# Kernel tuning notes

Hardware: AMD Instinct MI355X
Metric: run time of the kernel (lower is better)

The kernel has to match this reference:

```python
import jax, jax.numpy as jnp
import numpy as np
from jax import lax

B, C, H, W = 2, 64, 64, 64


def _conv1x1(x, w, b):
    # w: [Cout, Cin], x: [B, Cin, H, W]
    return jnp.einsum('oi,bihw->bohw', w, x) + b[None, :, None, None]


def _conv3x3(x, w, b):
    # w: [Cout, Cin, 3, 3]
    y = lax.conv_general_dilated(x, w, (1, 1), 'SAME',
                                 dimension_numbers=('NCHW', 'OIHW', 'NCHW'))
    return y + b[None, :, None, None]


def _bn(x, s, b, m, v, eps=1e-5):
    # eval-mode batchnorm with running stats
    inv = s / jnp.sqrt(v + eps)
    return x * inv[None, :, None, None] + (b - m * inv)[None, :, None, None]


def _prelu(x, a):
    return jnp.where(x > 0, x, a * x)


def _forward(x, g,
             pam_q_w, pam_q_b, pam_k_w, pam_k_b, pam_v_w, pam_v_b,
             pam_qg_w, pam_qg_b, pam_kg_w, pam_kg_b, gamma_p,
             se_fc1_w, se_fc2_w, gamma_c,
             pconv1_w, pconv1_b, pbn1_s, pbn1_b, pbn1_m, pbn1_v, pprelu1,
             pconv2_w, pconv2_b, pbn2_s, pbn2_b, pbn2_m, pbn2_v, pprelu2,
             cconv1_w, cconv1_b, cbn1_s, cbn1_b, cbn1_m, cbn1_v, cprelu1,
             cconv2_w, cconv2_b, cbn2_s, cbn2_b, cbn2_m, cbn2_v, cprelu2,
             fconv_w, fconv_b, fbn_s, fbn_b, fbn_m, fbn_v, fprelu):
    b, c, h, w = x.shape
    n = h * w
    sm = jax.nn.softmax
    # ---- G_PAM: position attention with guided double softmax ----
    q = _conv1x1(x, pam_q_w, pam_q_b).reshape(b, c, n)
    k = _conv1x1(x, pam_k_w, pam_k_b).reshape(b, c, n)
    v = _conv1x1(x, pam_v_w, pam_v_b).reshape(b, c, n)
    qg = _conv1x1(g, pam_qg_w, pam_qg_b).reshape(b, -1, n)
    kg = _conv1x1(g, pam_kg_w, pam_kg_b).reshape(b, -1, n)
    att = sm(jnp.einsum('bcn,bcm->bnm', q, k), axis=-1)        # [B,N,N]
    att_g = sm(jnp.einsum('bcn,bcm->bnm', qg, kg), axis=-1)    # [B,N,N]
    gatt = sm(jnp.einsum('bnk,bkm->bnm', att, att_g), axis=-1) # [B,N,N]
    pam_o = jnp.einsum('bcm,bnm->bcn', v, gatt).reshape(b, c, h, w)
    pam = gamma_p * pam_o + x
    # ---- pconv head ----
    t = _prelu(_bn(_conv3x3(pam, pconv1_w, pconv1_b), pbn1_s, pbn1_b, pbn1_m, pbn1_v), pprelu1)
    pam2 = _prelu(_bn(_conv1x1(t, pconv2_w, pconv2_b), pbn2_s, pbn2_b, pbn2_m, pbn2_v), pprelu2)
    # ---- G_CAM: channel attention with SE-gated guide ----
    xq = pam2.reshape(b, c, n)
    att_c = sm(jnp.einsum('bcn,bdn->bcd', xq, xq), axis=-1)    # [B,C,C]
    gy = g.mean((2, 3))  # SE: [B,C]
    gy = jax.nn.sigmoid(jnp.einsum('oc,bc->bo', se_fc2_w,
                                   jax.nn.relu(jnp.einsum('rc,bc->br', se_fc1_w, gy))))
    gq = (g * gy[:, :, None, None]).reshape(b, c, n)
    att_cg = sm(jnp.einsum('bcn,bdn->bcd', gq, gq), axis=-1)   # [B,C,C]
    ge = jnp.einsum('bck,bkd->bcd', att_c, att_cg)
    ge = jnp.max(ge, axis=-1, keepdims=True) - ge
    gatt_c = sm(ge, axis=-1)
    cam_o = jnp.einsum('bcd,bdn->bcn', gatt_c, xq).reshape(b, c, h, w)
    cam = gamma_c * cam_o + pam2
    # ---- cconv + fconv heads ----
    t = _prelu(_bn(_conv3x3(cam, cconv1_w, cconv1_b), cbn1_s, cbn1_b, cbn1_m, cbn1_v), cprelu1)
    cam2 = _prelu(_bn(_conv1x1(t, cconv2_w, cconv2_b), cbn2_s, cbn2_b, cbn2_m, cbn2_v), cprelu2)
    final = _prelu(_bn(_conv1x1(cam2, fconv_w, fconv_b), fbn_s, fbn_b, fbn_m, fbn_v), fprelu)
    return final


def setup_inputs() -> dict:
    key = jax.random.key(0)
    keys = iter(jax.random.split(key, 64))
    nk = lambda: next(keys)
    f32 = jnp.float32
    nrm = lambda shape, s=0.1: s * jax.random.normal(nk(), shape, f32)
    d = {}
    d['x'] = jax.random.normal(nk(), (B, C, H, W), f32)
    d['g'] = jax.random.normal(nk(), (B, C, H, W), f32)
    for p in ['pam_q', 'pam_k', 'pam_v', 'pam_qg', 'pam_kg']:
        d[p + '_w'] = nrm((C, C))
        d[p + '_b'] = nrm((C,))
    d['gamma_p'] = jnp.asarray(0.5, f32)
    d['se_fc1_w'] = nrm((C // 2, C))
    d['se_fc2_w'] = nrm((C, C // 2))
    d['gamma_c'] = jnp.asarray(0.5, f32)
    for pre in ['p', 'c']:
        d[pre + 'conv1_w'] = nrm((C, C, 3, 3), 0.05)
        d[pre + 'conv1_b'] = nrm((C,))
        d[pre + 'bn1_s'] = 1.0 + nrm((C,))
        d[pre + 'bn1_b'] = nrm((C,))
        d[pre + 'bn1_m'] = nrm((C,))
        d[pre + 'bn1_v'] = 1.0 + 0.1 * jax.random.uniform(nk(), (C,), f32)
        d[pre + 'prelu1'] = jnp.asarray(0.25, f32)
        d[pre + 'conv2_w'] = nrm((C, C))
        d[pre + 'conv2_b'] = nrm((C,))
        d[pre + 'bn2_s'] = 1.0 + nrm((C,))
        d[pre + 'bn2_b'] = nrm((C,))
        d[pre + 'bn2_m'] = nrm((C,))
        d[pre + 'bn2_v'] = 1.0 + 0.1 * jax.random.uniform(nk(), (C,), f32)
        d[pre + 'prelu2'] = jnp.asarray(0.25, f32)
    d['fconv_w'] = nrm((C, C))
    d['fconv_b'] = nrm((C,))
    d['fbn_s'] = 1.0 + nrm((C,))
    d['fbn_b'] = nrm((C,))
    d['fbn_m'] = nrm((C,))
    d['fbn_v'] = 1.0 + 0.1 * jax.random.uniform(nk(), (C,), f32)
    d['fprelu'] = jnp.asarray(0.25, f32)
    return d


def reference(x, g,
              pam_q_w, pam_q_b, pam_k_w, pam_k_b, pam_v_w, pam_v_b,
              pam_qg_w, pam_qg_b, pam_kg_w, pam_kg_b, gamma_p,
              se_fc1_w, se_fc2_w, gamma_c,
              pconv1_w, pconv1_b, pbn1_s, pbn1_b, pbn1_m, pbn1_v, pprelu1,
              pconv2_w, pconv2_b, pbn2_s, pbn2_b, pbn2_m, pbn2_v, pprelu2,
              cconv1_w, cconv1_b, cbn1_s, cbn1_b, cbn1_m, cbn1_v, cprelu1,
              cconv2_w, cconv2_b, cbn2_s, cbn2_b, cbn2_m, cbn2_v, cprelu2,
              fconv_w, fconv_b, fbn_s, fbn_b, fbn_m, fbn_v, fprelu):
    return _forward(x, g,
                    pam_q_w, pam_q_b, pam_k_w, pam_k_b, pam_v_w, pam_v_b,
                    pam_qg_w, pam_qg_b, pam_kg_w, pam_kg_b, gamma_p,
                    se_fc1_w, se_fc2_w, gamma_c,
                    pconv1_w, pconv1_b, pbn1_s, pbn1_b, pbn1_m, pbn1_v, pprelu1,
                    pconv2_w, pconv2_b, pbn2_s, pbn2_b, pbn2_m, pbn2_v, pprelu2,
                    cconv1_w, cconv1_b, cbn1_s, cbn1_b, cbn1_m, cbn1_v, cprelu1,
                    cconv2_w, cconv2_b, cbn2_s, cbn2_b, cbn2_m, cbn2_v, cprelu2,
                    fconv_w, fconv_b, fbn_s, fbn_b, fbn_m, fbn_v, fprelu)
```

## Files before the change

### kernel.cpp

```cpp
#include <hip/hip_runtime.h>
#include <hip/hip_fp8.h>


typedef float f32x4 __attribute__((ext_vector_type(4)));
typedef __bf16 bf16x8 __attribute__((ext_vector_type(8)));
typedef int int4v __attribute__((ext_vector_type(4)));
typedef int int8v __attribute__((ext_vector_type(8)));
typedef unsigned short ushort8 __attribute__((ext_vector_type(8)));
typedef unsigned char uchar8 __attribute__((ext_vector_type(8)));

#define DI __device__ __forceinline__

DI float bf2f(unsigned short u) { union { unsigned int i; float f; } x; x.i = ((unsigned int)u) << 16; return x.f; }
DI unsigned short f2bf(float f) { union { float f; unsigned int i; } x; x.f = f; unsigned int r = x.i + 0x7fff + ((x.i >> 16) & 1); return (unsigned short)(r >> 16); }
DI unsigned char f2fp8(float f) { __hip_fp8_e4m3 h(f); return (unsigned char)h.__x; }
DI float sane(float x) { return (x > -1e8f) ? ((x < 1e8f) ? x : 1e8f) : -1e8f; }

DI void async16(const unsigned short* g, unsigned short* l) {
    __builtin_amdgcn_global_load_lds(
        (const __attribute__((address_space(1))) void*)g,
        (__attribute__((address_space(3))) void*)l, 16, 0, 0);
}
DI void async16b(const unsigned char* g, unsigned char* l) {
    __builtin_amdgcn_global_load_lds(
        (const __attribute__((address_space(1))) void*)g,
        (__attribute__((address_space(3))) void*)l, 16, 0, 0);
}

__global__ __launch_bounds__(256) void diag_fill(float* __restrict__ out, int n, float val)
{
    int i = blockIdx.x * 256 + threadIdx.x;
    if (i < n) out[i] = val;
}

__global__ __launch_bounds__(256) void gemm_score(
    const unsigned short* __restrict__ A,
    const unsigned short* __restrict__ B,
    unsigned short* __restrict__ C, int N)
{
    const int tid  = threadIdx.x;
    const int bm   = blockIdx.y, bn = blockIdx.x;
    const int lane = tid & 63, wid = tid >> 6;
    const int wm   = (wid >> 1) * 64, wn = (wid & 1) * 64;
    const int l16  = lane & 15, quad = lane >> 4;

    f32x4 acc[4][4] = {};
    bf16x8 af[2][4], bfr[2][4];
    #pragma unroll
    for (int w = 0; w < 2; w++) {
        #pragma unroll
        for (int i = 0; i < 4; i++)
            af[w][i]  = *(const bf16x8*)&A[(long)(bm * 128 + wm + i * 16 + l16) * 64 + w * 32 + quad * 8];
        #pragma unroll
        for (int j = 0; j < 4; j++)
            bfr[w][j] = *(const bf16x8*)&B[(long)(bn * 128 + wn + j * 16 + l16) * 64 + w * 32 + quad * 8];
    }
    #pragma unroll
    for (int w = 0; w < 2; w++)
        #pragma unroll
        for (int i = 0; i < 4; i++)
            #pragma unroll
            for (int j = 0; j < 4; j++)
                acc[i][j] = __builtin_amdgcn_mfma_f32_16x16x32_bf16(af[w][i], bfr[w][j], acc[i][j], 0, 0, 0);

    #pragma unroll
    for (int i = 0; i < 4; i++) {
        int rb = bm * 128 + wm + i * 16 + quad * 4;
        #pragma unroll
        for (int j = 0; j < 4; j++) {
            int col = bn * 128 + wn + j * 16 + l16;
            #pragma unroll
            for (int r = 0; r < 4; r++)
                C[(long)(rb + r) * N + col] = f2bf(acc[i][j][r]);
        }
    }
}

__global__ __launch_bounds__(256, 3) void gemm_nt(
    const unsigned short* __restrict__ A,
    const unsigned short* __restrict__ B,
    float* __restrict__ C,
    int M, int N, int K)
{
    __shared__ __align__(16) unsigned short As[128 * 32];
    __shared__ __align__(16) unsigned short Bs[128 * 32];
    const int tid  = threadIdx.x;
    const int bm   = blockIdx.y, bn = blockIdx.x;
    const int lane = tid & 63, wid = tid >> 6;
    const int wm   = (wid >> 1) * 64, wn = (wid & 1) * 64;
    const int l16  = lane & 15, quad = lane >> 4;

    f32x4 acc[4][4] = {};

    const int Kc   = K / (int)gridDim.z;
    const int kbeg = (int)blockIdx.z * Kc;
    const int nIter = Kc / 32;

    const int row0 = tid >> 2,        cp0 = tid & 3;
    const int row1 = (tid + 256) >> 2, cp1 = (tid + 256) & 3;
    int ar0 = bm * 128 + row0; if (ar0 > M - 1) ar0 = M - 1;
    int ar1 = bm * 128 + row1; if (ar1 > M - 1) ar1 = M - 1;
    const unsigned short* pa0 = &A[(long)ar0 * K + kbeg + ((cp0 ^ (row0 & 3)) * 8)];
    const unsigned short* pa1 = &A[(long)ar1 * K + kbeg + ((cp1 ^ (row1 & 3)) * 8)];
    const unsigned short* pb0 = &B[(long)(bn * 128 + row0) * K + kbeg + ((cp0 ^ (row0 & 3)) * 8)];
    const unsigned short* pb1 = &B[(long)(bn * 128 + row1) * K + kbeg + ((cp1 ^ (row1 & 3)) * 8)];
    unsigned short* la0 = &As[row0 * 32 + cp0 * 8];
    unsigned short* la1 = &As[row1 * 32 + cp1 * 8];
    unsigned short* lb0 = &Bs[row0 * 32 + cp0 * 8];
    unsigned short* lb1 = &Bs[row1 * 32 + cp1 * 8];

    const int sw = (quad ^ (l16 & 3)) * 8;

    for (int it = 0; it < nIter; it++) {
        __syncthreads();
        async16(pa0, la0);
        async16(pa1, la1);
        async16(pb0, lb0);
        async16(pb1, lb1);
        pa0 += 32; pa1 += 32; pb0 += 32; pb1 += 32;
        __syncthreads();
        bf16x8 af[4], bfr[4];
        #pragma unroll
        for (int i = 0; i < 4; i++) af[i]  = *(const bf16x8*)&As[(wm + i * 16 + l16) * 32 + sw];
        #pragma unroll
        for (int j = 0; j < 4; j++) bfr[j] = *(const bf16x8*)&Bs[(wn + j * 16 + l16) * 32 + sw];
        #pragma unroll
        for (int i = 0; i < 4; i++)
            #pragma unroll
            for (int j = 0; j < 4; j++)
                acc[i][j] = __builtin_amdgcn_mfma_f32_16x16x32_bf16(af[i], bfr[j], acc[i][j], 0, 0, 0);
    }

    #pragma unroll
    for (int i = 0; i < 4; i++) {
        int rb = bm * 128 + wm + i * 16 + quad * 4;
        #pragma unroll
        for (int j = 0; j < 4; j++) {
            int col = bn * 128 + wn + j * 16 + l16;
            #pragma unroll
            for (int r = 0; r < 4; r++) {
                int row = rb + r;
                if (row < M)
                    C[(long)blockIdx.z * M * N + (long)row * N + col] = acc[i][j][r];
            }
        }
    }
}

__global__ __launch_bounds__(256, 3) void gemm_p8(
    const unsigned char* __restrict__ A,
    const unsigned char* __restrict__ B,
    unsigned short* __restrict__ C, int N, int K)
{
    __shared__ __align__(16) unsigned char As[128 * 128];
    __shared__ __align__(16) unsigned char Bs[128 * 128];
    const int tid  = threadIdx.x;
    const int bm   = blockIdx.y, bn = blockIdx.x;
    const int lane = tid & 63, wid = tid >> 6;
    const int wm   = (wid >> 1) * 64, wn = (wid & 1) * 64;
    const int l16  = lane & 15, quad = lane >> 4;

    f32x4 acc[4][4] = {};

    const unsigned char* pa[4];
    const unsigned char* pb[4];
    unsigned char* la[4];
    unsigned char* lb[4];
    #pragma unroll
    for (int m = 0; m < 4; m++) {
        int ch = tid + m * 256;
        int row = ch >> 3, sp = ch & 7;
        int cp = sp ^ (row & 7);
        pa[m] = &A[(long)(bm * 128 + row) * K + cp * 16];
        pb[m] = &B[(long)(bn * 128 + row) * K + cp * 16];
        la[m] = &As[row * 128 + sp * 16];
        lb[m] = &Bs[row * 128 + sp * 16];
    }

    const int s0 = ((2 * quad) ^ (l16 & 7)) * 16;
    const int s1 = ((2 * quad + 1) ^ (l16 & 7)) * 16;

    const int nIter = K / 128;
    for (int it = 0; it < nIter; it++) {
        __syncthreads();
        #pragma unroll
        for (int m = 0; m < 4; m++) {
            async16b(pa[m], la[m]);
            async16b(pb[m], lb[m]);
            pa[m] += 128; pb[m] += 128;
        }
        __syncthreads();
        int8v bfr[4];
        #pragma unroll
        for (int j = 0; j < 4; j++) {
            const unsigned char* base = &Bs[(wn + j * 16 + l16) * 128];
            int4v v0 = *(const int4v*)(base + s0);
            int4v v1 = *(const int4v*)(base + s1);
            bfr[j][0] = v0[0]; bfr[j][1] = v0[1]; bfr[j][2] = v0[2]; bfr[j][3] = v0[3];
            bfr[j][4] = v1[0]; bfr[j][5] = v1[1]; bfr[j][6] = v1[2]; bfr[j][7] = v1[3];
        }
        #pragma unroll
        for (int i = 0; i < 4; i++) {
            const unsigned char* base = &As[(wm + i * 16 + l16) * 128];
            int4v v0 = *(const int4v*)(base + s0);
            int4v v1 = *(const int4v*)(base + s1);
            int8v af;
            af[0] = v0[0]; af[1] = v0[1]; af[2] = v0[2]; af[3] = v0[3];
            af[4] = v1[0]; af[5] = v1[1]; af[6] = v1[2]; af[7] = v1[3];
            #pragma unroll
            for (int j = 0; j < 4; j++)
                acc[i][j] = __builtin_amdgcn_mfma_scale_f32_16x16x128_f8f6f4(
                    af, bfr[j], acc[i][j],
                    0, 0,
                    0, 0x7f7f7f7f,
                    0, 0x7f7f7f7f);
        }
    }

    const float ds = 1.f / 65536.f;
    #pragma unroll
    for (int i = 0; i < 4; i++) {
        int rb = bm * 128 + wm + i * 16 + quad * 4;
        #pragma unroll
        for (int j = 0; j < 4; j++) {
            int col = bn * 128 + wn + j * 16 + l16;
            #pragma unroll
            for (int r = 0; r < 4; r++)
                C[(long)(rb + r) * N + col] = f2bf(acc[i][j][r] * ds);
        }
    }
}

__global__ __launch_bounds__(256) void row_softmax(unsigned short* __restrict__ buf)
{
    long row = blockIdx.x;
    unsigned short* p = buf + row * 4096L;
    const int tid = threadIdx.x, lane = tid & 63, wid = tid >> 6;
    float v[16]; float mx = -1e30f;
    #pragma unroll
    for (int t = 0; t < 16; t++) {
        float x = sane(bf2f(p[t * 256 + tid]));
        v[t] = x; mx = fmaxf(mx, x);
    }
    #pragma unroll
    for (int o = 32; o; o >>= 1) mx = fmaxf(mx, __shfl_xor(mx, o, 64));
    __shared__ float rmax[4], rsum[4];
    if (!lane) rmax[wid] = mx;
    __syncthreads();
    mx = fmaxf(fmaxf(rmax[0], rmax[1]), fmaxf(rmax[2], rmax[3]));
    float s = 0.f;
    #pragma unroll
    for (int t = 0; t < 16; t++) { v[t] = __expf(v[t] - mx); s += v[t]; }
    #pragma unroll
    for (int o = 32; o; o >>= 1) s += __shfl_xor(s, o, 64);
    if (!lane) rsum[wid] = s;
    __syncthreads();
    s = rsum[0] + rsum[1] + rsum[2] + rsum[3];
    float inv = 1.f / s;
    #pragma unroll
    for (int t = 0; t < 16; t++) p[t * 256 + tid] = f2bf(v[t] * inv);
}

__global__ __launch_bounds__(256) void row_softmax_f8(
    const unsigned short* __restrict__ in, unsigned char* __restrict__ out)
{
    long row = blockIdx.x;
    const unsigned short* p = in + row * 4096L;
    unsigned char* q = out + row * 4096L;
    const int tid = threadIdx.x, lane = tid & 63, wid = tid >> 6;
    float v[16]; float mx = -1e30f;
    #pragma unroll
    for (int t = 0; t < 16; t++) {
        float x = sane(bf2f(p[t * 256 + tid]));
        v[t] = x; mx = fmaxf(mx, x);
    }
    #pragma unroll
    for (int o = 32; o; o >>= 1) mx = fmaxf(mx, __shfl_xor(mx, o, 64));
    __shared__ float rmax[4], rsum[4];
    if (!lane) rmax[wid] = mx;
    __syncthreads();
    mx = fmaxf(fmaxf(rmax[0], rmax[1]), fmaxf(rmax[2], rmax[3]));
    float s = 0.f;
    #pragma unroll
    for (int t = 0; t < 16; t++) { v[t] = __expf(v[t] - mx); s += v[t]; }
    #pragma unroll
    for (int o = 32; o; o >>= 1) s += __shfl_xor(s, o, 64);
    if (!lane) rsum[wid] = s;
    __syncthreads();
    s = rsum[0] + rsum[1] + rsum[2] + rsum[3];
    float inv = 256.f / s;
    #pragma unroll
    for (int t = 0; t < 16; t++) q[t * 256 + tid] = f2fp8(v[t] * inv);
}

__global__ __launch_bounds__(256) void colsm_partial(
    const unsigned short* __restrict__ buf,
    float* __restrict__ pmx, float* __restrict__ psum)
{
    const int tid = threadIdx.x;
    const int colgrp = tid & 63, rg = tid >> 6;
    const int cbase = blockIdx.x * 512 + colgrp * 8;
    const int r0 = blockIdx.y * 128 + rg * 32;
    const unsigned short* p = buf + (long)r0 * 4096 + cbase;
    float mx[8], s[8];
    #pragma unroll
    for (int j = 0; j < 8; j++) { mx[j] = -1e30f; s[j] = 0.f; }
    for (int r = 0; r < 32; r++) {
        ushort8 v = *(const ushort8*)(p + (long)r * 4096);
        #pragma unroll
        for (int j = 0; j < 8; j++) {
            float x = sane(bf2f(v[j]));
            float nm = fmaxf(mx[j], x);
            s[j] = s[j] * __expf(mx[j] - nm) + __expf(x - nm);
            mx[j] = nm;
        }
    }
    __shared__ float smx[4][512], ssm[4][512];
    #pragma unroll
    for (int j = 0; j < 8; j++) { smx[rg][colgrp * 8 + j] = mx[j]; ssm[rg][colgrp * 8 + j] = s[j]; }
    __syncthreads();
    for (int c = tid; c < 512; c += 256) {
        float M = fmaxf(fmaxf(smx[0][c], smx[1][c]), fmaxf(smx[2][c], smx[3][c]));
        float S = 0.f;
        #pragma unroll
        for (int i = 0; i < 4; i++) S += ssm[i][c] * __expf(smx[i][c] - M);
        int col = blockIdx.x * 512 + c;
        pmx[blockIdx.y * 4096 + col] = M;
        psum[blockIdx.y * 4096 + col] = S;
    }
}

__global__ __launch_bounds__(256) void colsm_combine(
    const float* __restrict__ pmx, const float* __restrict__ psum,
    float* __restrict__ gM, float* __restrict__ gInv)
{
    int col = blockIdx.x * 256 + threadIdx.x;
    float M = -1e30f;
    for (int ch = 0; ch < 32; ch++) M = fmaxf(M, pmx[ch * 4096 + col]);
    float S = 0.f;
    for (int ch = 0; ch < 32; ch++) S += psum[ch * 4096 + col] * __expf(pmx[ch * 4096 + col] - M);
    gM[col] = M;
    gInv[col] = 256.f / S;
}

__global__ __launch_bounds__(256) void colsm_norm_f8(
    const unsigned short* __restrict__ in, unsigned char* __restrict__ out,
    const float* __restrict__ gM, const float* __restrict__ gInv)
{
    const int tid = threadIdx.x;
    const int colgrp = tid & 63, rg = tid >> 6;
    const int cbase = blockIdx.x * 512 + colgrp * 8;
    const int r0 = blockIdx.y * 128 + rg * 32;
    const unsigned short* p = in + (long)r0 * 4096 + cbase;
    unsigned char* q = out + (long)r0 * 4096 + cbase;
    float M[8], inv[8];
    #pragma unroll
    for (int j = 0; j < 8; j++) { M[j] = gM[cbase + j]; inv[j] = gInv[cbase + j]; }
    for (int r = 0; r < 32; r++) {
        ushort8 v = *(const ushort8*)(p + (long)r * 4096);
        uchar8 o;
        #pragma unroll
        for (int j = 0; j < 8; j++) o[j] = f2fp8(__expf(sane(bf2f(v[j])) - M[j]) * inv[j]);
        *(uchar8*)(q + (long)r * 4096) = o;
    }
}

__global__ __launch_bounds__(256) void proj_nc(
    const float* __restrict__ X, const float* __restrict__ W,
    const float* __restrict__ bias, unsigned short* __restrict__ out)
{
    const int b = blockIdx.y, nt = blockIdx.x, tid = threadIdx.x;
    __shared__ float Xs[64][64];
    __shared__ float Ws[64][65];
    __shared__ float Bb[64];
    for (int f = tid; f < 4096; f += 256) {
        int i = f >> 6, n = f & 63;
        Xs[i][n] = X[((long)b * 64 + i) * 4096 + nt * 64 + n];
        Ws[f & 63][f >> 6] = W[f];
    }
    if (tid < 64) Bb[tid] = bias[tid];
    __syncthreads();
    const int c = tid & 63, g = tid >> 6;
    float acc[16];
    #pragma unroll
    for (int j = 0; j < 16; j++) acc[j] = Bb[c];
    for (int i = 0; i < 64; i++) {
        float wv = Ws[i][c];
        #pragma unroll
        for (int j = 0; j < 16; j++) acc[j] += wv * Xs[i][g + 4 * j];
    }
    unsigned short* ob = out + ((long)b * 4096 + nt * 64) * 64;
    #pragma unroll
    for (int j = 0; j < 16; j++) ob[(g + 4 * j) * 64 + c] = f2bf(acc[j]);
}

__global__ __launch_bounds__(256) void proj_cn(
    const float* __restrict__ X, const float* __restrict__ W,
    const float* __restrict__ bias, unsigned short* __restrict__ out)
{
    const int b = blockIdx.y, nt = blockIdx.x, tid = threadIdx.x;
    __shared__ float Xs[64][64];
    __shared__ float Ws[64][64];
    __shared__ float Bb[64];
    for (int f = tid; f < 4096; f += 256) {
        int i = f >> 6, n = f & 63;
        Xs[i][n] = X[((long)b * 64 + i) * 4096 + nt * 64 + n];
        Ws[f >> 6][f & 63] = W[f];
    }
    if (tid < 64) Bb[tid] = bias[tid];
    __syncthreads();
    const int n = tid & 63, g = tid >> 6;
    float acc[16];
    #pragma unroll
    for (int j = 0; j < 16; j++) acc[j] = Bb[g + 4 * j];
    for (int i = 0; i < 64; i++) {
        float xv = Xs[i][n];
        #pragma unroll
        for (int j = 0; j < 16; j++) acc[j] += Ws[g + 4 * j][i] * xv;
    }
    unsigned short* ob = out + ((long)b * 64) * 4096 + nt * 64;
    #pragma unroll
    for (int j = 0; j < 16; j++) ob[(long)(g + 4 * j) * 4096 + n] = f2bf(acc[j]);
}

__global__ __launch_bounds__(256) void combine_pam(
    const float* __restrict__ part, const float* __restrict__ x,
    const float* __restrict__ gammaPtr, float* __restrict__ pam, int nsplit)
{
    int i = blockIdx.x * 256 + threadIdx.x;
    float s = 0.f;
    for (int k = 0; k < nsplit; k++) s += part[(long)k * 262144 + i];
    pam[i] = gammaPtr[0] * s + x[i];
}

__global__ __launch_bounds__(256) void conv3x3_bn(
    const float* __restrict__ X, const float* __restrict__ W9,
    const float* __restrict__ bias,
    const float* __restrict__ bns, const float* __restrict__ bnb,
    const float* __restrict__ bnm, const float* __restrict__ bnv,
    const float* __restrict__ prelu, float* __restrict__ out)
{
    const int b = blockIdx.y, h = blockIdx.x, co0 = blockIdx.z * 16, tid = threadIdx.x;
    __shared__ float Ls[3][64][66];
    __shared__ float ep0[64], ep1[64], ep2[64];
    __shared__ float alpha;
    for (int f = tid; f < 3 * 64 * 64; f += 256) {
        int ky = f >> 12, rem = f & 4095, ci = rem >> 6, w = rem & 63;
        int hh = h + ky - 1;
        Ls[ky][ci][w + 1] = (hh >= 0 && hh < 64) ? X[(((long)b * 64 + ci) * 64 + hh) * 64 + w] : 0.f;
    }
    for (int f = tid; f < 192; f += 256) {
        int ky = f >> 6, ci = f & 63;
        Ls[ky][ci][0] = 0.f; Ls[ky][ci][65] = 0.f;
    }
    if (tid < 64) {
        float inv = bns[tid] * rsqrtf(fmaxf(bnv[tid], 0.f) + 1e-5f);
        ep0[tid] = inv; ep1[tid] = bnb[tid] - bnm[tid] * inv; ep2[tid] = bias[tid];
    }
    if (tid == 0) alpha = prelu[0];
    __syncthreads();
    const int w = tid & 63, g = tid >> 6;
    float acc[4];
    #pragma unroll
    for (int j = 0; j < 4; j++) acc[j] = ep2[co0 + g * 4 + j];
    for (int ci = 0; ci < 64; ci++) {
        float v0 = Ls[0][ci][w], v1 = Ls[0][ci][w + 1], v2 = Ls[0][ci][w + 2];
        float v3 = Ls[1][ci][w], v4 = Ls[1][ci][w + 1], v5 = Ls[1][ci][w + 2];
        float v6 = Ls[2][ci][w], v7 = Ls[2][ci][w + 1], v8 = Ls[2][ci][w + 2];
        #pragma unroll
        for (int j = 0; j < 4; j++) {
            const float* wp = &W9[((co0 + g * 4 + j) * 64 + ci) * 9];
            acc[j] += wp[0] * v0 + wp[1] * v1 + wp[2] * v2
                    + wp[3] * v3 + wp[4] * v4 + wp[5] * v5
                    + wp[6] * v6 + wp[7] * v7 + wp[8] * v8;
        }
    }
    #pragma unroll
    for (int j = 0; j < 4; j++) {
        int co = co0 + g * 4 + j;
        float y = acc[j] * ep0[co] + ep1[co];
        y = y > 0.f ? y : alpha * y;
        out[(((long)b * 64 + co) * 64 + h) * 64 + w] = y;
    }
}

__global__ __launch_bounds__(256) void conv1x1_bn(
    const float* __restrict__ X, const float* __restrict__ W,
    const float* __restrict__ bias,
    const float* __restrict__ bns, const float* __restrict__ bnb,
    const float* __restrict__ bnm, const float* __restrict__ bnv,
    const float* __restrict__ prelu, float* __restrict__ out)
{
    const int b = blockIdx.y, nt = blockIdx.x, tid = threadIdx.x;
    __shared__ float Xs[64][64];
    __shared__ float Ws[64][64];
    __shared__ float ep0[64], ep1[64], ep2[64];
    __shared__ float alpha;
    for (int f = tid; f < 4096; f += 256) {
        int i = f >> 6, n = f & 63;
        Xs[i][n] = X[((long)b * 64 + i) * 4096 + nt * 64 + n];
        Ws[f >> 6][f & 63] = W[f];
    }
    if (tid < 64) {
        float inv = bns[tid] * rsqrtf(fmaxf(bnv[tid], 0.f) + 1e-5f);
        ep0[tid] = inv; ep1[tid] = bnb[tid] - bnm[tid] * inv; ep2[tid] = bias[tid];
    }
    if (tid == 0) alpha = prelu[0];
    __syncthreads();
    const int n = tid & 63, g = tid >> 6;
    float acc[16];
    #pragma unroll
    for (int j = 0; j < 16; j++) acc[j] = ep2[g + 4 * j];
    for (int i = 0; i < 64; i++) {
        float xv = Xs[i][n];
        #pragma unroll
        for (int j = 0; j < 16; j++) acc[j] += Ws[g + 4 * j][i] * xv;
    }
    #pragma unroll
    for (int j = 0; j < 16; j++) {
        int c = g + 4 * j;
        float y = acc[j] * ep0[c] + ep1[c];
        y = y > 0.f ? y : alpha * y;
        out[((long)b * 64 + c) * 4096 + nt * 64 + n] = y;
    }
}

__global__ __launch_bounds__(256) void gram_partial(
    const float* __restrict__ X, float* __restrict__ out)
{
    const int ch = blockIdx.x, b = blockIdx.y, tid = threadIdx.x;
    __shared__ float Xs[64][65];
    for (int f = tid; f < 4096; f += 256) {
        int ci = f >> 6, kk = f & 63;
        Xs[ci][kk] = X[((long)b * 64 + ci) * 4096 + ch * 64 + kk];
    }
    __syncthreads();
    const int d = tid & 63, g = tid >> 6;
    float acc[16] = {};
    for (int kk = 0; kk < 64; kk++) {
        float xd = Xs[d][kk];
        #pragma unroll
        for (int j = 0; j < 16; j++) acc[j] += Xs[g + 4 * j][kk] * xd;
    }
    #pragma unroll
    for (int j = 0; j < 16; j++)
        atomicAdd(&out[((long)b * 64 + (g + 4 * j)) * 64 + d], acc[j]);
}

__global__ __launch_bounds__(256) void se_mean(
    const float* __restrict__ G, float* __restrict__ gy)
{
    const int c = blockIdx.x, b = blockIdx.y, tid = threadIdx.x;
    const int lane = tid & 63, wid = tid >> 6;
    const float* p = G + ((long)b * 64 + c) * 4096;
    float s = 0.f;
    #pragma unroll
    for (int t = 0; t < 4; t++) {
        f32x4 v = *(const f32x4*)(p + (t * 256 + tid) * 4);
        s += v[0] + v[1] + v[2] + v[3];
    }
    #pragma unroll
    for (int o = 32; o; o >>= 1) s += __shfl_xor(s, o, 64);
    __shared__ float ws[4];
    if (!lane) ws[wid] = s;
    __syncthreads();
    if (tid == 0) gy[b * 64 + c] = (ws[0] + ws[1] + ws[2] + ws[3]) * (1.f / 4096.f);
}

__global__ __launch_bounds__(64) void se_gate(
    const float* __restrict__ gy_in, const float* __restrict__ fc1,
    const float* __restrict__ fc2, float* __restrict__ gy2)
{
    const int b = blockIdx.x, tid = threadIdx.x;
    __shared__ float gy[64], r1[32];
    gy[tid] = gy_in[b * 64 + tid];
    __syncthreads();
    if (tid < 32) {
        float s = 0.f;
        for (int c = 0; c < 64; c++) s += fc1[tid * 64 + c] * gy[c];
        r1[tid] = fmaxf(s, 0.f);
    }
    __syncthreads();
    float s = 0.f;
    for (int r = 0; r < 32; r++) s += fc2[tid * 32 + r] * r1[r];
    gy2[b * 64 + tid] = 1.f / (1.f + __expf(-sane(s)));
}

__global__ __launch_bounds__(64) void cam_small(
    const float* __restrict__ gramx, const float* __restrict__ gramg,
    const float* __restrict__ gy2, float* __restrict__ gattc)
{
    const int b = blockIdx.x, tid = threadIdx.x;
    __shared__ float Ac[64][65], Acg[64][65];
    __shared__ float gys[64];
    gys[tid] = gy2[b * 64 + tid];
    __syncthreads();
    {
        const float* r = gramx + ((long)b * 64 + tid) * 64;
        float mx = -1e30f;
        for (int d = 0; d < 64; d++) mx = fmaxf(mx, sane(r[d]));
        float s = 0.f;
        for (int d = 0; d < 64; d++) s += __expf(sane(r[d]) - mx);
        float inv = 1.f / s;
        for (int d = 0; d < 64; d++) Ac[tid][d] = __expf(sane(r[d]) - mx) * inv;
    }
    {
        const float* r = gramg + ((long)b * 64 + tid) * 64;
        float gc = gys[tid];
        float mx = -1e30f;
        for (int d = 0; d < 64; d++) mx = fmaxf(mx, sane(gc * gys[d] * r[d]));
        float s = 0.f;
        for (int d = 0; d < 64; d++) s += __expf(sane(gc * gys[d] * r[d]) - mx);
        float inv = 1.f / s;
        for (int d = 0; d < 64; d++) Acg[tid][d] = __expf(sane(gc * gys[d] * r[d]) - mx) * inv;
    }
    __syncthreads();
    float ge[64];
    float mx1 = -1e30f, mn = 1e30f;
    for (int d = 0; d < 64; d++) {
        float s = 0.f;
        for (int k = 0; k < 64; k++) s += Ac[tid][k] * Acg[k][d];
        ge[d] = s;
        mx1 = fmaxf(mx1, s); mn = fminf(mn, s);
    }
    float M2 = mx1 - mn;
    float s = 0.f;
    for (int d = 0; d < 64; d++) s += __expf((mx1 - ge[d]) - M2);
    float inv = 1.f / s;
    for (int d = 0; d < 64; d++)
        gattc[((long)b * 64 + tid) * 64 + d] = __expf((mx1 - ge[d]) - M2) * inv;
}

__global__ __launch_bounds__(256) void cam_apply(
    const float* __restrict__ pam2, const float* __restrict__ gattc,
    const float* __restrict__ gammaPtr, float* __restrict__ cam)
{
    const int b = blockIdx.y, nt = blockIdx.x, tid = threadIdx.x;
    __shared__ float Xs[64][64];
    __shared__ float Gt[64][64];
    for (int f = tid; f < 4096; f += 256) {
        int d = f >> 6, n = f & 63;
        Xs[d][n] = pam2[((long)b * 64 + d) * 4096 + nt * 64 + n];
        Gt[f >> 6][f & 63] = gattc[((long)b * 64 + (f >> 6)) * 64 + (f & 63)];
    }
    __syncthreads();
    const float gamma = gammaPtr[0];
    const int n = tid & 63, g = tid >> 6;
    float acc[16] = {};
    for (int d = 0; d < 64; d++) {
        float xv = Xs[d][n];
        #pragma unroll
        for (int j = 0; j < 16; j++) acc[j] += Gt[g + 4 * j][d] * xv;
    }
    #pragma unroll
    for (int j = 0; j < 16; j++) {
        int c = g + 4 * j;
        cam[((long)b * 64 + c) * 4096 + nt * 64 + n] = gamma * acc[j] + Xs[c][n];
    }
}

extern "C" void kernel_launch(void* const* d_in, const int* in_sizes, int n_in,
                              void* d_out, int out_size, void* d_ws, size_t ws_size,
                              hipStream_t stream)
{
    static const int exp_sizes[51] = {
        524288, 524288,
        4096, 64, 4096, 64, 4096, 64, 4096, 64, 4096, 64,
        1, 2048, 2048, 1,
        36864, 64, 64, 64, 64, 64, 1,
        4096, 64, 64, 64, 64, 64, 1,
        36864, 64, 64, 64, 64, 64, 1,
        4096, 64, 64, 64, 64, 64, 1,
        4096, 64, 64, 64, 64, 64, 1
    };
    bool map_ok = (n_in == 51) && (out_size == 524288);
    if (map_ok) for (int i = 0; i < 51; i++) if (in_sizes[i] != exp_sizes[i]) { map_ok = false; break; }

    const int diag_grid = (out_size + 255) / 256;
    if (!map_ok) {
        diag_fill<<<diag_grid, 256, 0, stream>>>((float*)d_out, out_size, 400.0f);
        return;
    }
    const size_t NEED_FULL = 121000000;
    if (ws_size < NEED_FULL) {
        float code = (ws_size >= 88000000) ? 100.0f : (ws_size >= 55000000 ? 200.0f : 300.0f);
        diag_fill<<<diag_grid, 256, 0, stream>>>((float*)d_out, out_size, code);
        return;
    }

    auto IN = [&](int i) { return (const float*)d_in[i]; };
    const float* X = IN(0);
    const float* G = IN(1);

    char* wp_ = (char*)d_ws;
    auto alloc = [&](size_t bytes) -> void* {
        void* p = (void*)wp_;
        wp_ += (bytes + 255) & ~(size_t)255;
        return p;
    };
    unsigned short* qT   = (unsigned short*)alloc(2L * 4096 * 64 * 2);
    unsigned short* kT   = (unsigned short*)alloc(2L * 4096 * 64 * 2);
    unsigned short* qgT  = (unsigned short*)alloc(2L * 4096 * 64 * 2);
    unsigned short* kgT  = (unsigned short*)alloc(2L * 4096 * 64 * 2);
    unsigned short* vC   = (unsigned short*)alloc(2L * 64 * 4096 * 2);
    float* part  = (float*)alloc(8L * 64 * 4096 * 4);
    float* pam   = (float*)alloc(2L * 64 * 4096 * 4);
    float* tbuf  = (float*)alloc(2L * 64 * 4096 * 4);
    float* pam2  = (float*)alloc(2L * 64 * 4096 * 4);
    float* cam   = (float*)alloc(2L * 64 * 4096 * 4);
    float* gramx = (float*)alloc(2L * 64 * 64 * 4);
    float* gramg = (float*)alloc(2L * 64 * 64 * 4);
    float* gy    = (float*)alloc(2L * 64 * 4);
    float* gy2   = (float*)alloc(2L * 64 * 4);
    float* gattc = (float*)alloc(2L * 64 * 64 * 4);
    float* pmx   = (float*)alloc(32L * 4096 * 4);
    float* psum  = (float*)alloc(32L * 4096 * 4);
    float* gM    = (float*)alloc(4096L * 4);
    float* gInv  = (float*)alloc(4096L * 4);
    unsigned short* pbuf   = (unsigned short*)alloc(4096L * 4096 * 2);
    unsigned short* attS   = (unsigned short*)alloc(4096L * 4096 * 2);
    unsigned char*  attF8  = (unsigned char*)alloc(4096L * 4096);
    unsigned char*  attgF8 = (unsigned char*)alloc(4096L * 4096);
    float* cam2 = tbuf;

    proj_nc<<<dim3(64, 2), 256, 0, stream>>>(X, IN(2),  IN(3),  qT);
    proj_nc<<<dim3(64, 2), 256, 0, stream>>>(X, IN(4),  IN(5),  kT);
    proj_nc<<<dim3(64, 2), 256, 0, stream>>>(G, IN(8),  IN(9),  qgT);
    proj_nc<<<dim3(64, 2), 256, 0, stream>>>(G, IN(10), IN(11), kgT);
    proj_cn<<<dim3(64, 2), 256, 0, stream>>>(X, IN(6),  IN(7),  vC);

    for (int b = 0; b < 2; b++) {
        const unsigned short* qTb  = qT  + (long)b * 4096 * 64;
        const unsigned short* kTb  = kT  + (long)b * 4096 * 64;
        const unsigned short* qgTb = qgT + (long)b * 4096 * 64;
        const unsigned short* kgTb = kgT + (long)b * 4096 * 64;
        gemm_score<<<dim3(32, 32), 256, 0, stream>>>(qTb,  kTb,  pbuf, 4096);
        gemm_score<<<dim3(32, 32), 256, 0, stream>>>(kgTb, qgTb, attS, 4096);
        row_softmax_f8<<<4096, 256, 0, stream>>>(pbuf, attF8);
        colsm_partial<<<dim3(8, 32), 256, 0, stream>>>(attS, pmx, psum);
        colsm_combine<<<16, 256, 0, stream>>>(pmx, psum, gM, gInv);
        colsm_norm_f8<<<dim3(8, 32), 256, 0, stream>>>(attS, attgF8, gM, gInv);
        gemm_p8<<<dim3(32, 32), 256, 0, stream>>>(attF8, attgF8, pbuf, 4096, 4096);
        row_softmax<<<4096, 256, 0, stream>>>(pbuf);
        gemm_nt<<<dim3(32, 1, 8), 256, 0, stream>>>(vC + (long)b * 64 * 4096, pbuf, part,
                                                    64, 4096, 4096);
        combine_pam<<<1024, 256, 0, stream>>>(part, X + (long)b * 64 * 4096, IN(12),
                                              pam + (long)b * 64 * 4096, 8);
    }

    conv3x3_bn<<<dim3(64, 2, 4), 256, 0, stream>>>(pam, IN(16), IN(17), IN(18), IN(19), IN(20), IN(21), IN(22), tbuf);
    conv1x1_bn<<<dim3(64, 2), 256, 0, stream>>>(tbuf, IN(23), IN(24), IN(25), IN(26), IN(27), IN(28), IN(29), pam2);

    diag_fill<<<64, 256, 0, stream>>>(gramx, 16384, 0.0f);
    gram_partial<<<dim3(64, 2), 256, 0, stream>>>(pam2, gramx);
    gram_partial<<<dim3(64, 2), 256, 0, stream>>>(G,    gramg);
    se_mean<<<dim3(64, 2), 256, 0, stream>>>(G, gy);
    se_gate<<<2, 64, 0, stream>>>(gy, IN(13), IN(14), gy2);
    cam_small<<<2, 64, 0, stream>>>(gramx, gramg, gy2, gattc);
    cam_apply<<<dim3(64, 2), 256, 0, stream>>>(pam2, gattc, IN(15), cam);

    conv3x3_bn<<<dim3(64, 2, 4), 256, 0, stream>>>(cam, IN(30), IN(31), IN(32), IN(33), IN(34), IN(35), IN(36), pam);
    conv1x1_bn<<<dim3(64, 2), 256, 0, stream>>>(pam, IN(37), IN(38), IN(39), IN(40), IN(41), IN(42), IN(43), cam2);
    conv1x1_bn<<<dim3(64, 2), 256, 0, stream>>>(cam2, IN(44), IN(45), IN(46), IN(47), IN(48), IN(49), IN(50), (float*)d_out);
}
```

Measured before the change: 761.2 us.

## Batch both attention batches into single launches via grid z and fuse SE gate

Adds per-batch strides to the attention pipeline kernels so that both batch elements run in one launch, indexed by an extra grid dimension, when the workspace is large enough. This halves the number of launches and doubles the blocks per launch, which should improve GPU fill on small kernels such as colsm_combine and gemm_nt. The SE gate computation is also folded into cam_small, removing one tiny launch. The cost is doubled scratch buffers, with a fallback to the old per-batch loop when the workspace is too small.

```diff
diff --git a/kernel.cpp b/kernel.cpp
--- a/kernel.cpp
+++ b/kernel.cpp
@@ -36,8 +36,11 @@
 __global__ __launch_bounds__(256) void gemm_score(
     const unsigned short* __restrict__ A,
     const unsigned short* __restrict__ B,
-    unsigned short* __restrict__ C, int N)
-{
+    unsigned short* __restrict__ C, int N, long abStride, long cStride)
+{
+    A += (long)blockIdx.z * abStride;
+    B += (long)blockIdx.z * abStride;
+    C += (long)blockIdx.z * cStride;
     const int tid  = threadIdx.x;
     const int bm   = blockIdx.y, bn = blockIdx.x;
     const int lane = tid & 63, wid = tid >> 6;
@@ -80,26 +83,29 @@
     const unsigned short* __restrict__ A,
     const unsigned short* __restrict__ B,
     float* __restrict__ C,
-    int M, int N, int K)
-{
+    int M, int N, int K, long sA, long sB, long sC)
+{
+    A += (long)blockIdx.z * sA;
+    B += (long)blockIdx.z * sB;
+    C += (long)blockIdx.z * sC;
     __shared__ __align__(16) unsigned short As[128 * 32];
     __shared__ __align__(16) unsigned short Bs[128 * 32];
     const int tid  = threadIdx.x;
-    const int bm   = blockIdx.y, bn = blockIdx.x;
+    const int bn   = blockIdx.x, slice = blockIdx.y;
     const int lane = tid & 63, wid = tid >> 6;
     const int wm   = (wid >> 1) * 64, wn = (wid & 1) * 64;
     const int l16  = lane & 15, quad = lane >> 4;
 
     f32x4 acc[4][4] = {};
 
-    const int Kc   = K / (int)gridDim.z;
-    const int kbeg = (int)blockIdx.z * Kc;
+    const int Kc   = K / (int)gridDim.y;
+    const int kbeg = slice * Kc;
     const int nIter = Kc / 32;
 
     const int row0 = tid >> 2,        cp0 = tid & 3;
     const int row1 = (tid + 256) >> 2, cp1 = (tid + 256) & 3;
-    int ar0 = bm * 128 + row0; if (ar0 > M - 1) ar0 = M - 1;
-    int ar1 = bm * 128 + row1; if (ar1 > M - 1) ar1 = M - 1;
+    int ar0 = row0; if (ar0 > M - 1) ar0 = M - 1;
+    int ar1 = row1; if (ar1 > M - 1) ar1 = M - 1;
     const unsigned short* pa0 = &A[(long)ar0 * K + kbeg + ((cp0 ^ (row0 & 3)) * 8)];
     const unsigned short* pa1 = &A[(long)ar1 * K + kbeg + ((cp1 ^ (row1 & 3)) * 8)];
     const unsigned short* pb0 = &B[(long)(bn * 128 + row0) * K + kbeg + ((cp0 ^ (row0 & 3)) * 8)];
@@ -133,7 +139,7 @@
 
     #pragma unroll
     for (int i = 0; i < 4; i++) {
-        int rb = bm * 128 + wm + i * 16 + quad * 4;
+        int rb = wm + i * 16 + quad * 4;
         #pragma unroll
         for (int j = 0; j < 4; j++) {
             int col = bn * 128 + wn + j * 16 + l16;
@@ -141,7 +147,7 @@
             for (int r = 0; r < 4; r++) {
                 int row = rb + r;
                 if (row < M)
-                    C[(long)blockIdx.z * M * N + (long)row * N + col] = acc[i][j][r];
+                    C[(long)slice * M * N + (long)row * N + col] = acc[i][j][r];
             }
         }
     }
@@ -150,8 +156,12 @@
 __global__ __launch_bounds__(256, 3) void gemm_p8(
     const unsigned char* __restrict__ A,
     const unsigned char* __restrict__ B,
-    unsigned short* __restrict__ C, int N, int K)
-{
+    unsigned short* __restrict__ C, int N, int K,
+    long sA, long sB, long sC)
+{
+    A += (long)blockIdx.z * sA;
+    B += (long)blockIdx.z * sB;
+    C += (long)blockIdx.z * sC;
     __shared__ __align__(16) unsigned char As[128 * 128];
     __shared__ __align__(16) unsigned char Bs[128 * 128];
     const int tid  = threadIdx.x;
@@ -211,9 +221,7 @@
             for (int j = 0; j < 4; j++)
                 acc[i][j] = __builtin_amdgcn_mfma_scale_f32_16x16x128_f8f6f4(
                     af, bfr[j], acc[i][j],
-                    0, 0,
-                    0, 0x7f7f7f7f,
-                    0, 0x7f7f7f7f);
+                    0, 0, 0, 0x7f7f7f7f, 0, 0x7f7f7f7f);
         }
     }
 
@@ -231,10 +239,9 @@
     }
 }
 
-__global__ __launch_bounds__(256) void row_softmax(unsigned short* __restrict__ buf)
-{
-    long row = blockIdx.x;
-    unsigned short* p = buf + row * 4096L;
+__global__ __launch_bounds__(256) void row_softmax(unsigned short* __restrict__ buf, long bStride)
+{
+    unsigned short* p = buf + (long)blockIdx.y * bStride + (long)blockIdx.x * 4096;
     const int tid = threadIdx.x, lane = tid & 63, wid = tid >> 6;
     float v[16]; float mx = -1e30f;
     #pragma unroll
@@ -262,11 +269,11 @@
 }
 
 __global__ __launch_bounds__(256) void row_softmax_f8(
-    const unsigned short* __restrict__ in, unsigned char* __restrict__ out)
-{
-    long row = blockIdx.x;
-    const unsigned short* p = in + row * 4096L;
-    unsigned char* q = out + row * 4096L;
+    const unsigned short* __restrict__ in, unsigned char* __restrict__ out,
+    long inStride, long outStride)
+{
+    const unsigned short* p = in + (long)blockIdx.y * inStride + (long)blockIdx.x * 4096;
+    unsigned char* q = out + (long)blockIdx.y * outStride + (long)blockIdx.x * 4096;
     const int tid = threadIdx.x, lane = tid & 63, wid = tid >> 6;
     float v[16]; float mx = -1e30f;
     #pragma unroll
@@ -295,8 +302,12 @@
 
 __global__ __launch_bounds__(256) void colsm_partial(
     const unsigned short* __restrict__ buf,
-    float* __restrict__ pmx, float* __restrict__ psum)
-{
+    float* __restrict__ pmx, float* __restrict__ psum,
+    long bufStride, long pStride)
+{
+    buf  += (long)blockIdx.z * bufStride;
+    pmx  += (long)blockIdx.z * pStride;
+    psum += (long)blockIdx.z * pStride;
     const int tid = threadIdx.x;
     const int colgrp = tid & 63, rg = tid >> 6;
     const int cbase = blockIdx.x * 512 + colgrp * 8;
@@ -332,8 +343,13 @@
 
 __global__ __launch_bounds__(256) void colsm_combine(
     const float* __restrict__ pmx, const float* __restrict__ psum,
-    float* __restrict__ gM, float* __restrict__ gInv)
-{
+    float* __restrict__ gM, float* __restrict__ gInv,
+    long pStride, long gStride)
+{
+    pmx  += (long)blockIdx.y * pStride;
+    psum += (long)blockIdx.y * pStride;
+    gM   += (long)blockIdx.y * gStride;
+    gInv += (long)blockIdx.y * gStride;
     int col = blockIdx.x * 256 + threadIdx.x;
     float M = -1e30f;
     for (int ch = 0; ch < 32; ch++) M = fmaxf(M, pmx[ch * 4096 + col]);
@@ -345,8 +361,13 @@
 
 __global__ __launch_bounds__(256) void colsm_norm_f8(
     const unsigned short* __restrict__ in, unsigned char* __restrict__ out,
-    const float* __restrict__ gM, const float* __restrict__ gInv)
-{
+    const float* __restrict__ gM, const float* __restrict__ gInv,
+    long inStride, long outStride, long gStride)
+{
+    in   += (long)blockIdx.z * inStride;
+    out  += (long)blockIdx.z * outStride;
+    gM   += (long)blockIdx.z * gStride;
+    gInv += (long)blockIdx.z * gStride;
     const int tid = threadIdx.x;
     const int colgrp = tid & 63, rg = tid >> 6;
     const int cbase = blockIdx.x * 512 + colgrp * 8;
@@ -425,8 +446,12 @@
 
 __global__ __launch_bounds__(256) void combine_pam(
     const float* __restrict__ part, const float* __restrict__ x,
-    const float* __restrict__ gammaPtr, float* __restrict__ pam, int nsplit)
-{
+    const float* __restrict__ gammaPtr, float* __restrict__ pam, int nsplit,
+    long sPart, long sX)
+{
+    part += (long)blockIdx.y * sPart;
+    x    += (long)blockIdx.y * sX;
+    pam  += (long)blockIdx.y * sX;
     int i = blockIdx.x * 256 + threadIdx.x;
     float s = 0.f;
     for (int k = 0; k < nsplit; k++) s += part[(long)k * 262144 + i];
@@ -567,33 +592,27 @@
     if (tid == 0) gy[b * 64 + c] = (ws[0] + ws[1] + ws[2] + ws[3]) * (1.f / 4096.f);
 }
 
-__global__ __launch_bounds__(64) void se_gate(
+__global__ __launch_bounds__(64) void cam_small(
+    const float* __restrict__ gramx, const float* __restrict__ gramg,
     const float* __restrict__ gy_in, const float* __restrict__ fc1,
-    const float* __restrict__ fc2, float* __restrict__ gy2)
+    const float* __restrict__ fc2, float* __restrict__ gattc)
 {
     const int b = blockIdx.x, tid = threadIdx.x;
-    __shared__ float gy[64], r1[32];
-    gy[tid] = gy_in[b * 64 + tid];
+    __shared__ float Ac[64][65], Acg[64][65];
+    __shared__ float gyv[64], r1[32], gys[64];
+    gyv[tid] = gy_in[b * 64 + tid];
     __syncthreads();
     if (tid < 32) {
         float s = 0.f;
-        for (int c = 0; c < 64; c++) s += fc1[tid * 64 + c] * gy[c];
+        for (int c = 0; c < 64; c++) s += fc1[tid * 64 + c] * gyv[c];
         r1[tid] = fmaxf(s, 0.f);
     }
     __syncthreads();
-    float s = 0.f;
-    for (int r = 0; r < 32; r++) s += fc2[tid * 32 + r] * r1[r];
-    gy2[b * 64 + tid] = 1.f / (1.f + __expf(-sane(s)));
-}
-
-__global__ __launch_bounds__(64) void cam_small(
-    const float* __restrict__ gramx, const float* __restrict__ gramg,
-    const float* __restrict__ gy2, float* __restrict__ gattc)
-{
-    const int b = blockIdx.x, tid = threadIdx.x;
-    __shared__ float Ac[64][65], Acg[64][65];
-    __shared__ float gys[64];
-    gys[tid] = gy2[b * 64 + tid];
+    {
+        float s = 0.f;
+        for (int r = 0; r < 32; r++) s += fc2[tid * 32 + r] * r1[r];
+        gys[tid] = 1.f / (1.f + __expf(-sane(s)));
+    }
     __syncthreads();
     {
         const float* r = gramx + ((long)b * 64 + tid) * 64;
@@ -687,6 +706,9 @@
         diag_fill<<<diag_grid, 256, 0, stream>>>((float*)d_out, out_size, code);
         return;
     }
+    const bool big = (ws_size >= 248000000);
+    const int nb = big ? 2 : 1;
+    const long NN = 4096L * 4096;
 
     auto IN = [&](int i) { return (const float*)d_in[i]; };
     const float* X = IN(0);
@@ -703,7 +725,7 @@
     unsigned short* qgT  = (unsigned short*)alloc(2L * 4096 * 64 * 2);
     unsigned short* kgT  = (unsigned short*)alloc(2L * 4096 * 64 * 2);
     unsigned short* vC   = (unsigned short*)alloc(2L * 64 * 4096 * 2);
-    float* part  = (float*)alloc(8L * 64 * 4096 * 4);
+    float* part  = (float*)alloc((8L * nb) * 64 * 4096 * 4);
     float* pam   = (float*)alloc(2L * 64 * 4096 * 4);
     float* tbuf  = (float*)alloc(2L * 64 * 4096 * 4);
     float* pam2  = (float*)alloc(2L * 64 * 4096 * 4);
@@ -711,16 +733,15 @@
     float* gramx = (float*)alloc(2L * 64 * 64 * 4);
     float* gramg = (float*)alloc(2L * 64 * 64 * 4);
     float* gy    = (float*)alloc(2L * 64 * 4);
-    float* gy2   = (float*)alloc(2L * 64 * 4);
     float* gattc = (float*)alloc(2L * 64 * 64 * 4);
-    float* pmx   = (float*)alloc(32L * 4096 * 4);
-    float* psum  = (float*)alloc(32L * 4096 * 4);
-    float* gM    = (float*)alloc(4096L * 4);
-    float* gInv  = (float*)alloc(4096L * 4);
-    unsigned short* pbuf   = (unsigned short*)alloc(4096L * 4096 * 2);
-    unsigned short* attS   = (unsigned short*)alloc(4096L * 4096 * 2);
-    unsigned char*  attF8  = (unsigned char*)alloc(4096L * 4096);
-    unsigned char*  attgF8 = (unsigned char*)alloc(4096L * 4096);
+    float* pmx   = (float*)alloc((32L * nb) * 4096 * 4);
+    float* psum  = (float*)alloc((32L * nb) * 4096 * 4);
+    float* gM    = (float*)alloc(4096L * nb * 4);
+    float* gInv  = (float*)alloc(4096L * nb * 4);
+    unsigned short* pbuf   = (unsigned short*)alloc(NN * 2 * nb);
+    unsigned short* attS   = (unsigned short*)alloc(NN * 2 * nb);
+    unsigned char*  attF8  = (unsigned char*)alloc(NN * nb);
+    unsigned char*  attgF8 = (unsigned char*)alloc(NN * nb);
     float* cam2 = tbuf;
 
     proj_nc<<<dim3(64, 2), 256, 0, stream>>>(X, IN(2),  IN(3),  qT);
@@ -729,23 +750,30 @@
     proj_nc<<<dim3(64, 2), 256, 0, stream>>>(G, IN(10), IN(11), kgT);
     proj_cn<<<dim3(64, 2), 256, 0, stream>>>(X, IN(6),  IN(7),  vC);
 
-    for (int b = 0; b < 2; b++) {
-        const unsigned short* qTb  = qT  + (long)b * 4096 * 64;
-        const unsigned short* kTb  = kT  + (long)b * 4096 * 64;
-        const unsigned short* qgTb = qgT + (long)b * 4096 * 64;
-        const unsigned short* kgTb = kgT + (long)b * 4096 * 64;
-        gemm_score<<<dim3(32, 32), 256, 0, stream>>>(qTb,  kTb,  pbuf, 4096);
-        gemm_score<<<dim3(32, 32), 256, 0, stream>>>(kgTb, qgTb, attS, 4096);
-        row_softmax_f8<<<4096, 256, 0, stream>>>(pbuf, attF8);
-        colsm_partial<<<dim3(8, 32), 256, 0, stream>>>(attS, pmx, psum);
-        colsm_combine<<<16, 256, 0, stream>>>(pmx, psum, gM, gInv);
-        colsm_norm_f8<<<dim3(8, 32), 256, 0, stream>>>(attS, attgF8, gM, gInv);
-        gemm_p8<<<dim3(32, 32), 256, 0, stream>>>(attF8, attgF8, pbuf, 4096, 4096);
-        row_softmax<<<4096, 256, 0, stream>>>(pbuf);
-        gemm_nt<<<dim3(32, 1, 8), 256, 0, stream>>>(vC + (long)b * 64 * 4096, pbuf, part,
-                                                    64, 4096, 4096);
-        combine_pam<<<1024, 256, 0, stream>>>(part, X + (long)b * 64 * 4096, IN(12),
-                                              pam + (long)b * 64 * 4096, 8);
+    const long abStr = 4096L * 64;
+    const long pStr  = big ? NN : 0;
+    const long pmStr = big ? 32L * 4096 : 0;
+    const long gStr  = big ? 4096L : 0;
+    for (int b = 0; b < 2; b += nb) {
+        const unsigned short* qTb  = qT  + (long)b * abStr;
+        const unsigned short* kTb  = kT  + (long)b * abStr;
+        const unsigned short* qgTb = qgT + (long)b * abStr;
+        const unsigned short* kgTb = kgT + (long)b * abStr;
+        gemm_score<<<dim3(32, 32, nb), 256, 0, stream>>>(qTb,  kTb,  pbuf, 4096, abStr, pStr);
+        gemm_score<<<dim3(32, 32, nb), 256, 0, stream>>>(kgTb, qgTb, attS, 4096, abStr, pStr);
+        row_softmax_f8<<<dim3(4096, nb), 256, 0, stream>>>(pbuf, attF8, pStr, pStr);
+        colsm_partial<<<dim3(8, 32, nb), 256, 0, stream>>>(attS, pmx, psum, pStr, pmStr);
+        colsm_combine<<<dim3(16, nb), 256, 0, stream>>>(pmx, psum, gM, gInv, pmStr, gStr);
+        colsm_norm_f8<<<dim3(8, 32, nb), 256, 0, stream>>>(attS, attgF8, gM, gInv, pStr, pStr, gStr);
+        gemm_p8<<<dim3(32, 32, nb), 256, 0, stream>>>(attF8, attgF8, pbuf, 4096, 4096, pStr, pStr, pStr);
+        row_softmax<<<dim3(4096, nb), 256, 0, stream>>>(pbuf, pStr);
+        gemm_nt<<<dim3(32, 8, nb), 256, 0, stream>>>(vC + (long)b * abStr, pbuf, part,
+                                                     64, 4096, 4096,
+                                                     abStr, pStr, big ? 8L * 262144 : 0);
+        combine_pam<<<dim3(1024, nb), 256, 0, stream>>>(part, X + (long)b * 262144, IN(12),
+                                                        pam + (long)b * 262144, 8,
+                                                        big ? 8L * 262144 : 0,
+                                                        big ? 262144L : 0);
     }
 
     conv3x3_bn<<<dim3(64, 2, 4), 256, 0, stream>>>(pam, IN(16), IN(17), IN(18), IN(19), IN(20), IN(21), IN(22), tbuf);
@@ -755,8 +783,7 @@
     gram_partial<<<dim3(64, 2), 256, 0, stream>>>(pam2, gramx);
     gram_partial<<<dim3(64, 2), 256, 0, stream>>>(G,    gramg);
     se_mean<<<dim3(64, 2), 256, 0, stream>>>(G, gy);
-    se_gate<<<2, 64, 0, stream>>>(gy, IN(13), IN(14), gy2);
-    cam_small<<<2, 64, 0, stream>>>(gramx, gramg, gy2, gattc);
+    cam_small<<<2, 64, 0, stream>>>(gramx, gramg, gy, IN(13), IN(14), gattc);
     cam_apply<<<dim3(64, 2), 256, 0, stream>>>(pam2, gattc, IN(15), cam);
 
     conv3x3_bn<<<dim3(64, 2, 4), 256, 0, stream>>>(cam, IN(30), IN(31), IN(32), IN(33), IN(34), IN(35), IN(36), pam);
```

Measured after the change: 671.8 us. 11.7% less time.
